# Kernel tuning notes

Hardware: AMD Instinct MI355X
Metric: run time of the kernel (lower is better)

The kernel has to match this reference:

```python
import jax, jax.numpy as jnp
import numpy as np

N = 50000       # nodes
E = 800000      # edges (avg degree 16)
D_IN = 128      # input_dim
H = 64          # hidden_dim


def _lin(k, fan_in, fan_out):
    return jax.random.normal(k, (fan_in, fan_out), jnp.float32) / np.float32(np.sqrt(fan_in))


def setup_inputs() -> dict:
    key = jax.random.key(0)
    ks = jax.random.split(key, 12)
    x = jax.random.normal(ks[0], (N, D_IN), jnp.float32)
    edge_index = jax.random.randint(ks[1], (2, E), 0, N, dtype=jnp.int32)
    return {
        "x": x,
        "edge_index": edge_index,
        # GCN layers (weight stored [in, out]; bias added after aggregation, per PyG GCNConv)
        "W1": _lin(ks[2], D_IN, H), "b1": 0.01 * jax.random.normal(ks[3], (H,), jnp.float32),
        "W2": _lin(ks[4], H, H),    "b2": 0.01 * jax.random.normal(ks[5], (H,), jnp.float32),
        "W3": _lin(ks[6], H, H),    "b3": 0.01 * jax.random.normal(ks[7], (H,), jnp.float32),
        # MLP head. NOTE: concat(mean, max) has width 2*H, so fc1 is [2H, H].
        "fw1": _lin(ks[8], 2 * H, H), "fb1": 0.01 * jax.random.normal(ks[9], (H,), jnp.float32),
        "fw2": _lin(ks[10], H, 1),    "fb2": 0.01 * jax.random.normal(ks[11], (1,), jnp.float32),
    }


def _gcn(h_in, W, b, src, dst, dinv):
    # PyG GCNConv: h = X W; out_i = sum_j norm_ij * h_j over in-edges + self-loop + bias
    h = h_in @ W                                   # [N, out]
    norm = (dinv[src] * dinv[dst])[:, None]        # [E, 1]
    msg = h[src] * norm                            # [E, out] gather + scale
    agg = jax.ops.segment_sum(msg, dst, num_segments=N)
    agg = agg + (dinv * dinv)[:, None] * h + b     # self-loop contribution + bias
    return agg


def reference(x, edge_index, W1, b1, W2, b2, W3, b3, fw1, fb1, fw2, fb2):
    src, dst = edge_index[0], edge_index[1]
    # degree including self-loops (counted on target nodes, PyG default)
    deg = jax.ops.segment_sum(jnp.ones((E,), x.dtype), dst, num_segments=N) + 1.0
    dinv = jax.lax.rsqrt(deg)

    h = jax.nn.relu(_gcn(x, W1, b1, src, dst, dinv))
    h = jax.nn.relu(_gcn(h, W2, b2, src, dst, dinv))
    h = jax.nn.relu(_gcn(h, W3, b3, src, dst, dinv))

    pooled = jnp.concatenate([jnp.mean(h, axis=0, keepdims=True),
                              jnp.max(h, axis=0, keepdims=True)], axis=1)  # [1, 2H]
    out = jax.nn.relu(pooled @ fw1 + fb1) @ fw2 + fb2                       # [1, 1]
    return out
```

## Files before the change

### kernel.cpp

```cpp
#include <hip/hip_runtime.h>
#include <math.h>


typedef _Float16 h8 __attribute__((ext_vector_type(8)));
typedef _Float16 half8 __attribute__((ext_vector_type(8)));

__global__ __launch_bounds__(256) void zero_kernel(int* __restrict__ degc,
                                                   float* __restrict__ psum,
                                                   unsigned int* __restrict__ pmax, int n) {
  int i = blockIdx.x * 256 + threadIdx.x;
  if (i < n) degc[i] = 0;
  if (blockIdx.x == 0 && threadIdx.x < 64) {
    psum[threadIdx.x] = 0.0f;
    pmax[threadIdx.x] = 0u;
  }
}

__global__ __launch_bounds__(256) void hist_kernel(const int* __restrict__ dst,
                                                   int* __restrict__ degc, int E) {
  int e = blockIdx.x * 256 + threadIdx.x;
  if (e < E) atomicAdd(&degc[dst[e]], 1);
}

__global__ __launch_bounds__(256) void scanA_kernel(const int* __restrict__ deg,
                                                    int* __restrict__ bsum, int n) {
  __shared__ int sdata[256];
  int t = threadIdx.x;
  int i = blockIdx.x * 256 + t;
  sdata[t] = (i < n) ? deg[i] : 0;
  __syncthreads();
  for (int off = 128; off > 0; off >>= 1) {
    if (t < off) sdata[t] += sdata[t + off];
    __syncthreads();
  }
  if (t == 0) bsum[blockIdx.x] = sdata[0];
}

__global__ __launch_bounds__(256) void scanB_kernel(int* __restrict__ bsum, int nb) {
  __shared__ int s[256];
  int t = threadIdx.x;
  int v = (t < nb) ? bsum[t] : 0;
  s[t] = v;
  __syncthreads();
  for (int off = 1; off < 256; off <<= 1) {
    int x = (t >= off) ? s[t - off] : 0;
    __syncthreads();
    s[t] += x;
    __syncthreads();
  }
  if (t < nb) bsum[t] = s[t] - v;
}

__global__ __launch_bounds__(256) void scanC_kernel(const int* __restrict__ deg,
                                                    const int* __restrict__ bsum,
                                                    int* __restrict__ rowptr,
                                                    float* __restrict__ dinv,
                                                    int* __restrict__ bkt_cur,
                                                    int n, int e_total) {
  __shared__ int s[256];
  int t = threadIdx.x;
  int i = blockIdx.x * 256 + t;
  int v = (i < n) ? deg[i] : 0;
  s[t] = v;
  __syncthreads();
  for (int off = 1; off < 256; off <<= 1) {
    int x = (t >= off) ? s[t - off] : 0;
    __syncthreads();
    s[t] += x;
    __syncthreads();
  }
  if (i < n) {
    int excl = bsum[blockIdx.x] + s[t] - v;
    rowptr[i] = excl;
    dinv[i] = 1.0f / sqrtf((float)v + 1.0f);
    if ((i & 255) == 0) bkt_cur[i >> 8] = excl;
  }
  if (i == 0) rowptr[n] = e_total;
}

__global__ __launch_bounds__(256) void binA_kernel(const int* __restrict__ src,
                                                   const int* __restrict__ dst,
                                                   int* __restrict__ bkt_cur,
                                                   int* __restrict__ binned, int E) {
  __shared__ int hist[256];
  __shared__ int scan[256];
  __shared__ int delta[256];
  __shared__ int lcur[256];
  __shared__ int sorted[4096];
  __shared__ unsigned char bkt_of[4096];
  const int t = threadIdx.x;
  hist[t] = 0;
  __syncthreads();
  const int e0 = blockIdx.x * 4096;
  int pk[16];
  int bk[16];
#pragma unroll
  for (int i = 0; i < 16; ++i) {
    int e = e0 + t + 256 * i;
    if (e < E) {
      int s_ = src[e], d_ = dst[e];
      int b = d_ >> 8;
      pk[i] = (s_ << 8) | (d_ & 255);
      bk[i] = b;
      atomicAdd(&hist[b], 1);
    } else {
      bk[i] = -1;
    }
  }
  __syncthreads();
  int v = hist[t];
  scan[t] = v;
  __syncthreads();
  for (int off = 1; off < 256; off <<= 1) {
    int x = (t >= off) ? scan[t - off] : 0;
    __syncthreads();
    scan[t] += x;
    __syncthreads();
  }
  int excl = scan[t] - v;
  int g = (v > 0) ? atomicAdd(&bkt_cur[t], v) : 0;
  delta[t] = g - excl;
  lcur[t] = excl;
  __syncthreads();
#pragma unroll
  for (int i = 0; i < 16; ++i) {
    if (bk[i] >= 0) {
      int p = atomicAdd(&lcur[bk[i]], 1);
      sorted[p] = pk[i];
      bkt_of[p] = (unsigned char)bk[i];
    }
  }
  __syncthreads();
  const int tot = scan[255];
  for (int i = t; i < tot; i += 256)
    binned[delta[bkt_of[i]] + i] = sorted[i];
}

__global__ __launch_bounds__(256) void binB_kernel(const int* __restrict__ rowptr,
                                                   const int* __restrict__ binned,
                                                   int* __restrict__ csr_src, int n) {
  __shared__ int lcur[256];
  const int t = threadIdx.x;
  const int base = blockIdx.x << 8;
  const int rbeg = rowptr[base];
  const int node = base + t;
  lcur[t] = (node < n) ? rowptr[node] - rbeg : 0;
  const int nend = (base + 256 < n) ? base + 256 : n;
  const int rend = rowptr[nend];
  const int cnt = rend - rbeg;
  __syncthreads();
  for (int i = t; i < cnt; i += 256) {
    int e = binned[rbeg + i];
    int p = atomicAdd(&lcur[e & 255], 1);
    csr_src[rbeg + p] = e >> 8;
  }
}

template <int K>
__global__ __launch_bounds__(256) void mm_kernel(const float* __restrict__ A,
                                                 const float* __restrict__ W,
                                                 const float* __restrict__ dinv,
                                                 _Float16* __restrict__ C, int nrows) {
  __shared__ float As[64 * K];
  const int t = threadIdx.x;
  const int lane = t & 63;
  const int wid = __builtin_amdgcn_readfirstlane(t >> 6);
  const int row0 = blockIdx.x * 64;

  constexpr int F4_PER_ROW = K / 4;
  constexpr int ROW_SHIFT = (K == 128) ? 5 : 4;
#pragma unroll
  for (int i = 0; i < K / 16; ++i) {
    int e4 = t + 256 * i;
    int r = e4 >> ROW_SHIFT;
    int k = (e4 & (F4_PER_ROW - 1)) * 4;
    int rc = row0 + r;
    if (rc > nrows - 1) rc = nrows - 1;
    float4 v = *(const float4*)(A + (size_t)rc * K + k);
    int s = r & 31;
    As[r * K + ((k + 0) ^ s)] = v.x;
    As[r * K + ((k + 1) ^ s)] = v.y;
    As[r * K + ((k + 2) ^ s)] = v.z;
    As[r * K + ((k + 3) ^ s)] = v.w;
  }
  __syncthreads();

  const int colbase = wid * 16;
  const float* Wc = W + colbase;
  float acc[16];
#pragma unroll
  for (int j = 0; j < 16; ++j) acc[j] = 0.0f;
  const int sw = lane & 31;
  const float* Arow = As + lane * K;

#pragma unroll 8
  for (int k = 0; k < K; ++k) {
    float a = Arow[k ^ sw];
    const float* Wk = Wc + k * 64;
#pragma unroll
    for (int j = 0; j < 16; ++j) acc[j] = fmaf(a, Wk[j], acc[j]);
  }

  int row = row0 + lane;
  if (row < nrows) {
    float dv = dinv[row];
    _Float16* Crow = C + (size_t)row * 64 + colbase;
    half8 o0, o1;
#pragma unroll
    for (int q = 0; q < 8; ++q) o0[q] = (_Float16)(dv * acc[q]);
#pragma unroll
    for (int q = 0; q < 8; ++q) o1[q] = (_Float16)(dv * acc[8 + q]);
    *(half8*)(Crow + 0) = o0;
    *(half8*)(Crow + 8) = o1;
  }
}

__global__ __launch_bounds__(256) void agg_kernel(const _Float16* __restrict__ hp,
                                                  const int* __restrict__ rowptr,
                                                  const int* __restrict__ csr_src,
                                                  const float* __restrict__ dinv,
                                                  const float* __restrict__ bias,
                                                  float* __restrict__ out, int n) {
  const int t = threadIdx.x;
  const int lane = t & 63;
  const int g = lane >> 3;
  const int s = lane & 7;
  const int wid = __builtin_amdgcn_readfirstlane(t >> 6);
  const int node = blockIdx.x * 4 + wid;
  if (node >= n) return;
  const int rbeg = rowptr[node];
  const int rend = rowptr[node + 1];
  const int deg = rend - rbeg;
  const int nbf = deg >> 3;
  const int rem = deg & 7;

  float a0, a1, a2, a3, a4, a5, a6, a7;
  {
    h8 v = *(const h8*)(hp + ((size_t)node << 6) + (s << 3));
    float m = (g == 0) ? 1.0f : 0.0f;
    a0 = m * (float)v[0]; a1 = m * (float)v[1];
    a2 = m * (float)v[2]; a3 = m * (float)v[3];
    a4 = m * (float)v[4]; a5 = m * (float)v[5];
    a6 = m * (float)v[6]; a7 = m * (float)v[7];
  }

  int j = rbeg;
#pragma unroll 2
  for (int b = 0; b < nbf; ++b, j += 8) {
    int i0 = csr_src[j + 0], i1 = csr_src[j + 1], i2 = csr_src[j + 2], i3 = csr_src[j + 3];
    int i4 = csr_src[j + 4], i5 = csr_src[j + 5], i6 = csr_src[j + 6], i7 = csr_src[j + 7];
    int idx = (g & 4) ? ((g & 2) ? ((g & 1) ? i7 : i6) : ((g & 1) ? i5 : i4))
                      : ((g & 2) ? ((g & 1) ? i3 : i2) : ((g & 1) ? i1 : i0));
    h8 v = *(const h8*)(hp + ((size_t)idx << 6) + (s << 3));
    a0 += (float)v[0]; a1 += (float)v[1];
    a2 += (float)v[2]; a3 += (float)v[3];
    a4 += (float)v[4]; a5 += (float)v[5];
    a6 += (float)v[6]; a7 += (float)v[7];
  }
  if (rem) {
    int i0 = csr_src[j + 0];
    int i1 = (rem > 1) ? csr_src[j + 1] : i0;
    int i2 = (rem > 2) ? csr_src[j + 2] : i0;
    int i3 = (rem > 3) ? csr_src[j + 3] : i0;
    int i4 = (rem > 4) ? csr_src[j + 4] : i0;
    int i5 = (rem > 5) ? csr_src[j + 5] : i0;
    int i6 = (rem > 6) ? csr_src[j + 6] : i0;
    int idx = (g & 4) ? ((g & 2) ? ((g & 1) ? i0 : i6) : ((g & 1) ? i5 : i4))
                      : ((g & 2) ? ((g & 1) ? i3 : i2) : ((g & 1) ? i1 : i0));
    h8 v = *(const h8*)(hp + ((size_t)idx << 6) + (s << 3));
    float w = (g < rem) ? 1.0f : 0.0f;
    a0 = fmaf(w, (float)v[0], a0); a1 = fmaf(w, (float)v[1], a1);
    a2 = fmaf(w, (float)v[2], a2); a3 = fmaf(w, (float)v[3], a3);
    a4 = fmaf(w, (float)v[4], a4); a5 = fmaf(w, (float)v[5], a5);
    a6 = fmaf(w, (float)v[6], a6); a7 = fmaf(w, (float)v[7], a7);
  }

  a0 += __shfl_xor(a0, 8); a0 += __shfl_xor(a0, 16); a0 += __shfl_xor(a0, 32);
  a1 += __shfl_xor(a1, 8); a1 += __shfl_xor(a1, 16); a1 += __shfl_xor(a1, 32);
  a2 += __shfl_xor(a2, 8); a2 += __shfl_xor(a2, 16); a2 += __shfl_xor(a2, 32);
  a3 += __shfl_xor(a3, 8); a3 += __shfl_xor(a3, 16); a3 += __shfl_xor(a3, 32);
  a4 += __shfl_xor(a4, 8); a4 += __shfl_xor(a4, 16); a4 += __shfl_xor(a4, 32);
  a5 += __shfl_xor(a5, 8); a5 += __shfl_xor(a5, 16); a5 += __shfl_xor(a5, 32);
  a6 += __shfl_xor(a6, 8); a6 += __shfl_xor(a6, 16); a6 += __shfl_xor(a6, 32);
  a7 += __shfl_xor(a7, 8); a7 += __shfl_xor(a7, 16); a7 += __shfl_xor(a7, 32);

  if (g == 0) {
    const float dv = dinv[node];
    const float* bp = bias + (s << 3);
    float4 b0 = *(const float4*)(bp + 0);
    float4 b1 = *(const float4*)(bp + 4);
    float4 r0, r1;
    r0.x = fmaxf(fmaf(dv, a0, b0.x), 0.0f);
    r0.y = fmaxf(fmaf(dv, a1, b0.y), 0.0f);
    r0.z = fmaxf(fmaf(dv, a2, b0.z), 0.0f);
    r0.w = fmaxf(fmaf(dv, a3, b0.w), 0.0f);
    r1.x = fmaxf(fmaf(dv, a4, b1.x), 0.0f);
    r1.y = fmaxf(fmaf(dv, a5, b1.y), 0.0f);
    r1.z = fmaxf(fmaf(dv, a6, b1.z), 0.0f);
    r1.w = fmaxf(fmaf(dv, a7, b1.w), 0.0f);
    float* op = out + ((size_t)node << 6) + (s << 3);
    *(float4*)(op + 0) = r0;
    *(float4*)(op + 4) = r1;
  }
}

__global__ __launch_bounds__(256) void pool_kernel(const float* __restrict__ gbuf,
                                                   float* __restrict__ psum,
                                                   unsigned int* __restrict__ pmax, int n) {
  __shared__ float ls[4][64];
  __shared__ float lm[4][64];
  const int lane = threadIdx.x & 63;
  const int wid = threadIdx.x >> 6;
  const int stride = 256 * 4;
  float s = 0.0f, m = 0.0f;
  for (int base = blockIdx.x * 4 + wid; base < n; base += 4 * stride) {
#pragma unroll
    for (int k = 0; k < 4; ++k) {
      int node = base + k * stride;
      if (node < n) {
        float v = gbuf[((size_t)node << 6) + lane];
        s += v;
        m = fmaxf(m, v);
      }
    }
  }
  ls[wid][lane] = s;
  lm[wid][lane] = m;
  __syncthreads();
  if (wid == 0) {
    for (int w = 1; w < 4; ++w) {
      s += ls[w][lane];
      m = fmaxf(m, lm[w][lane]);
    }
    atomicAdd(&psum[lane], s);
    atomicMax(&pmax[lane], __float_as_uint(m));
  }
}

__global__ __launch_bounds__(64) void head_kernel(const float* __restrict__ psum,
                                                  const float* __restrict__ pmaxf,
                                                  const float* __restrict__ fw1,
                                                  const float* __restrict__ fb1,
                                                  const float* __restrict__ fw2,
                                                  const float* __restrict__ fb2,
                                                  float* __restrict__ out, float invN) {
  int lane = threadIdx.x;
  float acc = fb1[lane];
#pragma unroll 4
  for (int k = 0; k < 64; ++k)
    acc = fmaf(psum[k] * invN, fw1[k * 64 + lane], acc);
#pragma unroll 4
  for (int k = 0; k < 64; ++k)
    acc = fmaf(pmaxf[k], fw1[(64 + k) * 64 + lane], acc);
  float a = fmaxf(acc, 0.0f) * fw2[lane];
  for (int off = 32; off > 0; off >>= 1) a += __shfl_down(a, off);
  if (lane == 0) out[0] = a + fb2[0];
}

extern "C" void kernel_launch(void* const* d_in, const int* in_sizes, int n_in,
                              void* d_out, int out_size, void* d_ws, size_t ws_size,
                              hipStream_t stream) {
  const float* x   = (const float*)d_in[0];
  const int*   ei  = (const int*)d_in[1];
  const float* W1  = (const float*)d_in[2];
  const float* b1  = (const float*)d_in[3];
  const float* W2  = (const float*)d_in[4];
  const float* b2  = (const float*)d_in[5];
  const float* W3  = (const float*)d_in[6];
  const float* b3  = (const float*)d_in[7];
  const float* fw1 = (const float*)d_in[8];
  const float* fb1 = (const float*)d_in[9];
  const float* fw2 = (const float*)d_in[10];
  const float* fb2 = (const float*)d_in[11];
  float* out = (float*)d_out;

  const int N = in_sizes[0] / 128;
  const int E = in_sizes[1] / 2;
  const int* src = ei;
  const int* dst = ei + E;

  char* ws = (char*)d_ws;
  size_t off = 0;
  auto alloc = [&](size_t bytes) -> char* {
    char* p = ws + off;
    off = (off + bytes + 255) & ~(size_t)255;
    return p;
  };
  float*        dinv    = (float*)alloc((size_t)N * 4);
  int*          degc    = (int*)alloc((size_t)N * 4);
  int*          rowptr  = (int*)alloc((size_t)(N + 1) * 4);
  int*          bsum    = (int*)alloc(256 * 4);
  int*          bkt_cur = (int*)alloc(256 * 4);
  int*          binned  = (int*)alloc((size_t)E * 4 + 64);
  int*          csr_src = (int*)alloc((size_t)E * 4 + 64);
  _Float16*     bufA    = (_Float16*)alloc((size_t)N * 64 * 2);
  float*        bufB    = (float*)alloc((size_t)N * 64 * 4);
  float*        psum    = (float*)alloc(64 * 4);
  unsigned int* pmax    = (unsigned int*)alloc(64 * 4);

  const int histBlk = (E + 255) / 256;
  const int scanBlk = (N + 255) / 256;
  const int mmBlk   = (N + 63) / 64;
  const int aggBlk  = (N + 3) / 4;
  const int NB      = (N + 255) / 256;
  const int binBlk  = (E + 4095) / 4096;

  zero_kernel<<<scanBlk, 256, 0, stream>>>(degc, psum, pmax, N);
  hist_kernel<<<histBlk, 256, 0, stream>>>(dst, degc, E);
  scanA_kernel<<<scanBlk, 256, 0, stream>>>(degc, bsum, N);
  scanB_kernel<<<1, 256, 0, stream>>>(bsum, scanBlk);
  scanC_kernel<<<scanBlk, 256, 0, stream>>>(degc, bsum, rowptr, dinv, bkt_cur, N, E);
  binA_kernel<<<binBlk, 256, 0, stream>>>(src, dst, bkt_cur, binned, E);
  binB_kernel<<<NB, 256, 0, stream>>>(rowptr, binned, csr_src, N);

  mm_kernel<128><<<mmBlk, 256, 0, stream>>>(x, W1, dinv, bufA, N);
  agg_kernel<<<aggBlk, 256, 0, stream>>>(bufA, rowptr, csr_src, dinv, b1, bufB, N);
  mm_kernel<64><<<mmBlk, 256, 0, stream>>>(bufB, W2, dinv, bufA, N);
  agg_kernel<<<aggBlk, 256, 0, stream>>>(bufA, rowptr, csr_src, dinv, b2, bufB, N);
  mm_kernel<64><<<mmBlk, 256, 0, stream>>>(bufB, W3, dinv, bufA, N);
  agg_kernel<<<aggBlk, 256, 0, stream>>>(bufA, rowptr, csr_src, dinv, b3, bufB, N);

  pool_kernel<<<256, 256, 0, stream>>>(bufB, psum, pmax, N);
  head_kernel<<<1, 64, 0, stream>>>(psum, (const float*)pmax, fw1, fb1, fw2, fb2, out,
                                    1.0f / (float)N);
}
```

Baseline: 303.5 us.

## Replace per-node degree histogram and scans with coarse bucket histogram

Instead of atomically counting each node's in-degree and doing a three-kernel global scan, a small grid counts edges per 256-node bucket in shared memory. A single block scans the bucket totals. The binning pass then computes per-node degrees, rowptr and dinv locally in shared memory for each bucket. This removes 800K global atomics and several launches, at the cost of an extra pass over the binned array inside each bucket block.

```diff
diff --git a/kernel.cpp b/kernel.cpp
--- a/kernel.cpp
+++ b/kernel.cpp
@@ -5,41 +5,28 @@
 typedef _Float16 h8 __attribute__((ext_vector_type(8)));
 typedef _Float16 half8 __attribute__((ext_vector_type(8)));
 
-__global__ __launch_bounds__(256) void zero_kernel(int* __restrict__ degc,
-                                                   float* __restrict__ psum,
-                                                   unsigned int* __restrict__ pmax, int n) {
-  int i = blockIdx.x * 256 + threadIdx.x;
-  if (i < n) degc[i] = 0;
-  if (blockIdx.x == 0 && threadIdx.x < 64) {
-    psum[threadIdx.x] = 0.0f;
-    pmax[threadIdx.x] = 0u;
-  }
-}
-
-__global__ __launch_bounds__(256) void hist_kernel(const int* __restrict__ dst,
-                                                   int* __restrict__ degc, int E) {
-  int e = blockIdx.x * 256 + threadIdx.x;
-  if (e < E) atomicAdd(&degc[dst[e]], 1);
-}
-
-__global__ __launch_bounds__(256) void scanA_kernel(const int* __restrict__ deg,
-                                                    int* __restrict__ bsum, int n) {
-  __shared__ int sdata[256];
-  int t = threadIdx.x;
-  int i = blockIdx.x * 256 + t;
-  sdata[t] = (i < n) ? deg[i] : 0;
-  __syncthreads();
-  for (int off = 128; off > 0; off >>= 1) {
-    if (t < off) sdata[t] += sdata[t + off];
-    __syncthreads();
-  }
-  if (t == 0) bsum[blockIdx.x] = sdata[0];
-}
-
-__global__ __launch_bounds__(256) void scanB_kernel(int* __restrict__ bsum, int nb) {
+__global__ __launch_bounds__(256) void cnt_kernel(const int* __restrict__ dst,
+                                                  int* __restrict__ bucket_hist, int E) {
+  __shared__ int h[256];
+  const int t = threadIdx.x;
+  h[t] = 0;
+  __syncthreads();
+  for (int e = blockIdx.x * 256 + t; e < E; e += gridDim.x * 256)
+    atomicAdd(&h[dst[e] >> 8], 1);
+  __syncthreads();
+  if (h[t]) atomicAdd(&bucket_hist[t], h[t]);
+}
+
+__global__ __launch_bounds__(256) void scan196_kernel(const int* __restrict__ bucket_hist,
+                                                      int* __restrict__ bkt_cur,
+                                                      int* __restrict__ bkt_base,
+                                                      int* __restrict__ rowptr,
+                                                      float* __restrict__ psum,
+                                                      unsigned int* __restrict__ pmax,
+                                                      int nb, int n, int E) {
   __shared__ int s[256];
-  int t = threadIdx.x;
-  int v = (t < nb) ? bsum[t] : 0;
+  const int t = threadIdx.x;
+  int v = (t < nb) ? bucket_hist[t] : 0;
   s[t] = v;
   __syncthreads();
   for (int off = 1; off < 256; off <<= 1) {
@@ -48,34 +35,17 @@
     s[t] += x;
     __syncthreads();
   }
-  if (t < nb) bsum[t] = s[t] - v;
-}
-
-__global__ __launch_bounds__(256) void scanC_kernel(const int* __restrict__ deg,
-                                                    const int* __restrict__ bsum,
-                                                    int* __restrict__ rowptr,
-                                                    float* __restrict__ dinv,
-                                                    int* __restrict__ bkt_cur,
-                                                    int n, int e_total) {
-  __shared__ int s[256];
-  int t = threadIdx.x;
-  int i = blockIdx.x * 256 + t;
-  int v = (i < n) ? deg[i] : 0;
-  s[t] = v;
-  __syncthreads();
-  for (int off = 1; off < 256; off <<= 1) {
-    int x = (t >= off) ? s[t - off] : 0;
-    __syncthreads();
-    s[t] += x;
-    __syncthreads();
-  }
-  if (i < n) {
-    int excl = bsum[blockIdx.x] + s[t] - v;
-    rowptr[i] = excl;
-    dinv[i] = 1.0f / sqrtf((float)v + 1.0f);
-    if ((i & 255) == 0) bkt_cur[i >> 8] = excl;
-  }
-  if (i == 0) rowptr[n] = e_total;
+  int base = s[t] - v;
+  if (t < nb) {
+    bkt_cur[t] = base;
+    bkt_base[t] = base;
+  }
+  if (t == nb) bkt_base[nb] = E;
+  if (t == 0) rowptr[n] = E;
+  if (t < 64) {
+    psum[t] = 0.0f;
+    pmax[t] = 0u;
+  }
 }
 
 __global__ __launch_bounds__(256) void binA_kernel(const int* __restrict__ src,
@@ -136,23 +106,43 @@
     binned[delta[bkt_of[i]] + i] = sorted[i];
 }
 
-__global__ __launch_bounds__(256) void binB_kernel(const int* __restrict__ rowptr,
+__global__ __launch_bounds__(256) void binC_kernel(const int* __restrict__ bkt_base,
                                                    const int* __restrict__ binned,
+                                                   int* __restrict__ rowptr,
+                                                   float* __restrict__ dinv,
                                                    int* __restrict__ csr_src, int n) {
+  __shared__ int lh[256];
+  __shared__ int ls[256];
   __shared__ int lcur[256];
   const int t = threadIdx.x;
-  const int base = blockIdx.x << 8;
-  const int rbeg = rowptr[base];
-  const int node = base + t;
-  lcur[t] = (node < n) ? rowptr[node] - rbeg : 0;
-  const int nend = (base + 256 < n) ? base + 256 : n;
-  const int rend = rowptr[nend];
-  const int cnt = rend - rbeg;
+  const int b = blockIdx.x;
+  const int base = bkt_base[b];
+  const int cnt = bkt_base[b + 1] - base;
+  lh[t] = 0;
+  __syncthreads();
+  for (int i = t; i < cnt; i += 256) atomicAdd(&lh[binned[base + i] & 255], 1);
+  __syncthreads();
+  const int deg = lh[t];
+  ls[t] = deg;
+  __syncthreads();
+  for (int off = 1; off < 256; off <<= 1) {
+    int x = (t >= off) ? ls[t - off] : 0;
+    __syncthreads();
+    ls[t] += x;
+    __syncthreads();
+  }
+  const int excl = ls[t] - deg;
+  const int node = (b << 8) + t;
+  if (node < n) {
+    rowptr[node] = base + excl;
+    dinv[node] = 1.0f / sqrtf((float)deg + 1.0f);
+  }
+  lcur[t] = excl;
   __syncthreads();
   for (int i = t; i < cnt; i += 256) {
-    int e = binned[rbeg + i];
+    int e = binned[base + i];
     int p = atomicAdd(&lcur[e & 255], 1);
-    csr_src[rbeg + p] = e >> 8;
+    csr_src[base + p] = e >> 8;
   }
 }
 
@@ -386,32 +376,29 @@
     off = (off + bytes + 255) & ~(size_t)255;
     return p;
   };
-  float*        dinv    = (float*)alloc((size_t)N * 4);
-  int*          degc    = (int*)alloc((size_t)N * 4);
-  int*          rowptr  = (int*)alloc((size_t)(N + 1) * 4);
-  int*          bsum    = (int*)alloc(256 * 4);
-  int*          bkt_cur = (int*)alloc(256 * 4);
-  int*          binned  = (int*)alloc((size_t)E * 4 + 64);
-  int*          csr_src = (int*)alloc((size_t)E * 4 + 64);
-  _Float16*     bufA    = (_Float16*)alloc((size_t)N * 64 * 2);
-  float*        bufB    = (float*)alloc((size_t)N * 64 * 4);
-  float*        psum    = (float*)alloc(64 * 4);
-  unsigned int* pmax    = (unsigned int*)alloc(64 * 4);
-
-  const int histBlk = (E + 255) / 256;
-  const int scanBlk = (N + 255) / 256;
-  const int mmBlk   = (N + 63) / 64;
-  const int aggBlk  = (N + 3) / 4;
-  const int NB      = (N + 255) / 256;
-  const int binBlk  = (E + 4095) / 4096;
-
-  zero_kernel<<<scanBlk, 256, 0, stream>>>(degc, psum, pmax, N);
-  hist_kernel<<<histBlk, 256, 0, stream>>>(dst, degc, E);
-  scanA_kernel<<<scanBlk, 256, 0, stream>>>(degc, bsum, N);
-  scanB_kernel<<<1, 256, 0, stream>>>(bsum, scanBlk);
-  scanC_kernel<<<scanBlk, 256, 0, stream>>>(degc, bsum, rowptr, dinv, bkt_cur, N, E);
+  float*        dinv     = (float*)alloc((size_t)N * 4);
+  int*          rowptr   = (int*)alloc((size_t)(N + 1) * 4);
+  int*          bhist    = (int*)alloc(256 * 4);
+  int*          bkt_cur  = (int*)alloc(256 * 4);
+  int*          bkt_base = (int*)alloc(257 * 4);
+  int*          binned   = (int*)alloc((size_t)E * 4 + 64);
+  int*          csr_src  = (int*)alloc((size_t)E * 4 + 64);
+  _Float16*     bufA     = (_Float16*)alloc((size_t)N * 64 * 2);
+  float*        bufB     = (float*)alloc((size_t)N * 64 * 4);
+  float*        psum     = (float*)alloc(64 * 4);
+  unsigned int* pmax     = (unsigned int*)alloc(64 * 4);
+
+  const int mmBlk  = (N + 63) / 64;
+  const int aggBlk = (N + 3) / 4;
+  const int NB     = (N + 255) / 256;
+  const int binBlk = (E + 4095) / 4096;
+
+  hipMemsetAsync(bhist, 0, 256 * 4, stream);
+  cnt_kernel<<<128, 256, 0, stream>>>(dst, bhist, E);
+  scan196_kernel<<<1, 256, 0, stream>>>(bhist, bkt_cur, bkt_base, rowptr, psum, pmax,
+                                        NB, N, E);
   binA_kernel<<<binBlk, 256, 0, stream>>>(src, dst, bkt_cur, binned, E);
-  binB_kernel<<<NB, 256, 0, stream>>>(rowptr, binned, csr_src, N);
+  binC_kernel<<<NB, 256, 0, stream>>>(bkt_base, binned, rowptr, dinv, csr_src, N);
 
   mm_kernel<128><<<mmBlk, 256, 0, stream>>>(x, W1, dinv, bufA, N);
   agg_kernel<<<aggBlk, 256, 0, stream>>>(bufA, rowptr, csr_src, dinv, b1, bufB, N);
```

New measurement: 274.6 us. 9.6% less time.
